# Optimization experiments

Measured on AMD Instinct MI355X. Metric: run time of the kernel, lower is better.

## Reference

```python
import jax, jax.numpy as jnp
import numpy as np

N, E = 16384, 262144
NS_N, NV_N = 128, 64      # node irreps: 128x0e + 64x1o
NS_E, NV_E = 64, 32       # edge irreps: 64x0e + 32x1o
C_OH, LAT = 16, 128
DS, DV = 128, 64          # irreps_out: 128x0e + 64x1o
GS = DS + DV              # gate input scalars (128 act scalars + 64 gates)
SC = 2 * NS_N + NS_E      # 320 concatenated scalar channels
VC = 2 * NV_N + NV_E      # 160 concatenated l=1 channels
M0_IN = SC + VC           # 480 m=0 features into SO2 linear
M0_OUT = GS + DV          # 256 m=0 outputs
AVG_NEI = 16.0
EPS = 1e-8


def setup_inputs() -> dict:
    key = jax.random.key(0)
    ks = jax.random.split(key, 20)
    f = lambda k, s: jax.random.normal(k, s, dtype=jnp.float32)
    return dict(
        node_feat=f(ks[0], (N, NS_N + 3 * NV_N)),
        edge_feat=f(ks[1], (E, NS_E + 3 * NV_E)),
        edge_vec=f(ks[2], (E, 3)),
        latents=f(ks[3], (E, LAT)),
        node_onehot=jax.nn.one_hot(jax.random.randint(ks[4], (N,), 0, C_OH), C_OH, dtype=jnp.float32),
        ln_n_g0=jnp.ones(NS_N), ln_n_b0=jnp.zeros(NS_N), ln_n_g1=jnp.ones(NV_N),
        ln_e_g0=jnp.ones(NS_E), ln_e_b0=jnp.zeros(NS_E), ln_e_g1=jnp.ones(NV_E),
        W_m0=f(ks[5], (M0_IN, M0_OUT)),
        w_r=f(ks[6], (VC, DV)), w_i=f(ks[7], (VC, DV)),
        W_env=f(ks[8], (LAT, DS + DV)),
        Wp0=f(ks[9], (DS, DS)), bp0=jnp.zeros(DS), Wpv=f(ks[10], (DV, DV)),
        Wtp0=f(ks[11], (DS, C_OH, GS)), Wtp1=f(ks[12], (DV, C_OH, DV)),
        Wo0=f(ks[13], (DS, DS)), bo0=jnp.zeros(DS), Wov=f(ks[14], (DV, DV)),
        res_param=jnp.zeros(()),
        edge_index=jax.random.randint(ks[15], (2, E), 0, N),
    )


def _sep_ln(s, v, g0, b0, g1):
    # separable equivariant layer norm: LN on scalars, per-sample RMS on l=1 block
    mu = s.mean(-1, keepdims=True)
    var = jnp.mean((s - mu) ** 2, -1, keepdims=True)
    s = (s - mu) * jax.lax.rsqrt(var + EPS) * g0 + b0
    vvar = jnp.mean(v * v, axis=(-2, -1), keepdims=True)  # component norm, degree-balanced (single l=1)
    v = v * jax.lax.rsqrt(vvar + EPS) * g1[None, :, None]
    return s, v


def _edge_frame(vec):
    # orthonormal frame (a, e1, e2) with a along the edge
    a = vec * jax.lax.rsqrt(jnp.sum(vec * vec, -1, keepdims=True) + EPS)
    helper = jnp.where(jnp.abs(a[:, 2:3]) < 0.99,
                       jnp.array([0.0, 0.0, 1.0], dtype=vec.dtype),
                       jnp.array([1.0, 0.0, 0.0], dtype=vec.dtype))
    e1 = jnp.cross(helper, a)
    e1 = e1 * jax.lax.rsqrt(jnp.sum(e1 * e1, -1, keepdims=True) + EPS)
    e2 = jnp.cross(a, e1)
    return a, e1, e2


def reference(node_feat, edge_feat, edge_vec, latents, node_onehot,
              ln_n_g0, ln_n_b0, ln_n_g1, ln_e_g0, ln_e_b0, ln_e_g1,
              W_m0, w_r, w_i, W_env, Wp0, bp0, Wpv,
              Wtp0, Wtp1, Wo0, bo0, Wov, res_param, edge_index):
    src, dst = edge_index[0], edge_index[1]
    ns, nv = node_feat[:, :NS_N], node_feat[:, NS_N:].reshape(-1, NV_N, 3)
    es, ev = edge_feat[:, :NS_E], edge_feat[:, NS_E:].reshape(-1, NV_E, 3)
    ns, nv = _sep_ln(ns, nv, ln_n_g0, ln_n_b0, ln_n_g1)
    es, ev = _sep_ln(es, ev, ln_e_g0, ln_e_b0, ln_e_g1)
    # per-edge concat: node[src] + edge + node[dst]
    s_cat = jnp.concatenate([ns[src], es, ns[dst]], -1)          # [E, SC]
    v_cat = jnp.concatenate([nv[src], ev, nv[dst]], 1)           # [E, VC, 3]
    # SO2 linear: rotate into edge frame, mix per |m|, rotate back
    a, e1, e2 = _edge_frame(edge_vec)
    c0 = jnp.einsum('eci,ei->ec', v_cat, a)
    c1 = jnp.einsum('eci,ei->ec', v_cat, e1)
    c2 = jnp.einsum('eci,ei->ec', v_cat, e2)
    m0 = jnp.concatenate([s_cat, c0], -1) @ W_m0 * (1.0 / np.sqrt(M0_IN))  # [E, M0_OUT]
    s_out, c0o = m0[:, :GS], m0[:, GS:]
    inv = 1.0 / np.sqrt(VC)
    c1o = (c1 @ w_r - c2 @ w_i) * inv
    c2o = (c1 @ w_i + c2 @ w_r) * inv
    v_out = (c0o[..., None] * a[:, None, :] + c1o[..., None] * e1[:, None, :]
             + c2o[..., None] * e2[:, None, :])                  # [E, DV, 3]
    # gate activation
    s_act = jax.nn.silu(s_out[:, :DS])
    gates = jax.nn.sigmoid(s_out[:, DS:])
    v_g = v_out * gates[..., None]
    # lin_post (per-l linear, scalar bias)
    s2 = s_act @ Wp0 * (1.0 / np.sqrt(DS)) + bp0
    v2 = jnp.einsum('eui,uv->evi', v_g, Wpv) * (1.0 / np.sqrt(DV))
    # env weighting from latents (E3ElementLinear, per-irrep-channel scalars)
    w = latents @ W_env * (1.0 / np.sqrt(LAT))
    s2 = s2 * w[:, :DS]
    v2 = v2 * w[:, DS:, None]
    nrm = 1.0 / np.sqrt(AVG_NEI)
    sa = jax.ops.segment_sum(s2, dst, num_segments=N) * nrm
    va = jax.ops.segment_sum(v2, dst, num_segments=N) * nrm
    # one-hot FullyConnectedTensorProduct (in2 all 0e) + gate + linear
    t0 = jnp.einsum('nu,nc,ucv->nv', sa, node_onehot, Wtp0) * (1.0 / np.sqrt(DS * C_OH))
    t1 = jnp.einsum('nui,nc,ucv->nvi', va, node_onehot, Wtp1) * (1.0 / np.sqrt(DV * C_OH))
    s3 = jax.nn.silu(t0[:, :DS])
    v3 = t1 * jax.nn.sigmoid(t0[:, DS:])[..., None]
    s4 = s3 @ Wo0 * (1.0 / np.sqrt(DS)) + bo0
    v4 = jnp.einsum('nui,uv->nvi', v3, Wov) * (1.0 / np.sqrt(DV))
    new = jnp.concatenate([s4, v4.reshape(-1, 3 * DV)], -1)
    r = jax.nn.sigmoid(res_param)
    return r * node_feat + (1.0 - r) * new
```

## Files before the change

### kernel.cpp

```cpp
#include <hip/hip_runtime.h>
#include <math.h>

#define N_NODES 16384
#define N_EDGES 262144
#define EPSF 1e-8f

#define OFF_X     0
#define OFF_C12   31232
#define OFF_LAT   52224
#define OFF_FR    60928
#define OFF_EDST  62464
#define OFF_WENV  62592
#define POOL_BYTES 75392
#define OFF_SACT  0
#define OFF_GATE  8704
#define OFF_C0O   17408
#define OFF_C1O   31232
#define OFF_C2O   39936
#define OFF_VG    8704

typedef __bf16 bf16x8 __attribute__((ext_vector_type(8)));
typedef float  f32x4  __attribute__((ext_vector_type(4)));

__device__ __forceinline__ f32x4 MFMA16(bf16x8 a, bf16x8 b, f32x4 c){
  return __builtin_amdgcn_mfma_f32_16x16x32_bf16(a, b, c, 0, 0, 0);
}

__device__ __forceinline__ unsigned short f2bf(float x){
  union { float f; unsigned u; } c; c.f = x;
  unsigned u = c.u;
  u += 0x7FFFu + ((u>>16)&1u);
  return (unsigned short)(u>>16);
}
__device__ __forceinline__ float bf2f(unsigned short h){
  union { unsigned u; float f; } c; c.u = ((unsigned)h)<<16;
  return c.f;
}
__device__ __forceinline__ float wsum64(float v){
  #pragma unroll
  for (int m=1; m<64; m<<=1) v += __shfl_xor(v, m);
  return v;
}
__device__ __forceinline__ float wsum32(float v){
  #pragma unroll
  for (int m=1; m<32; m<<=1) v += __shfl_xor(v, m);
  return v;
}
__device__ __forceinline__ float sigm(float x){ return 1.0f/(1.0f+__expf(-x)); }
__device__ __forceinline__ float silu(float x){ return x/(1.0f+__expf(-x)); }

__global__ __launch_bounds__(256) void k_pack(const float* __restrict__ src,
                                              unsigned short* __restrict__ dst,
                                              int K, int N){
  int i = blockIdx.x*256 + threadIdx.x;
  if (i >= K*N) return;
  int k = i / N, n = i - k*N;
  int idx = (((k>>5)*N + n)*4 + ((k>>3)&3))*8 + (k&7);
  dst[idx] = f2bf(src[i]);
}
__global__ __launch_bounds__(256) void k_pack_wc(const float* __restrict__ wr,
                                                 const float* __restrict__ wi,
                                                 unsigned short* __restrict__ dst){
  int i = blockIdx.x*256 + threadIdx.x;
  if (i >= 320*128) return;
  int k = i >> 7, n = i & 127;
  float v;
  if (k < 160) v = (n < 64) ? wr[k*64 + n]        : wi[k*64 + (n-64)];
  else         v = (n < 64) ? -wi[(k-160)*64 + n] : wr[(k-160)*64 + (n-64)];
  int idx = (((k>>5)*128 + n)*4 + ((k>>3)&3))*8 + (k&7);
  dst[idx] = f2bf(v);
}

__global__ __launch_bounds__(256) void k_hist(const int* __restrict__ eidx, int* __restrict__ cnt){
  int e = blockIdx.x*256 + threadIdx.x;
  if (e < N_EDGES) atomicAdd(&cnt[eidx[N_EDGES+e]], 1);
}
__global__ __launch_bounds__(256) void k_scan(const int* __restrict__ cnt,
                                              int* __restrict__ rowp, int* __restrict__ cursor){
  __shared__ int part[256];
  __shared__ int pref[257];
  const int t = threadIdx.x;
  const int base = t*64;
  int s = 0;
  for (int i=0;i<64;i++) s += cnt[base+i];
  part[t] = s; __syncthreads();
  if (t==0){ int a=0; for (int i=0;i<256;i++){ pref[i]=a; a+=part[i]; } pref[256]=a; }
  __syncthreads();
  int a = pref[t];
  for (int i=0;i<64;i++){ rowp[base+i]=a; cursor[base+i]=a; a += cnt[base+i]; }
  if (t==0) rowp[N_NODES] = pref[256];
}
__global__ __launch_bounds__(256) void k_fill(const int* __restrict__ eidx,
                                              int* __restrict__ cursor, int* __restrict__ perm){
  int e = blockIdx.x*256 + threadIdx.x;
  if (e < N_EDGES){
    int pos = atomicAdd(&cursor[eidx[N_EDGES+e]], 1);
    perm[pos] = e;
  }
}

__global__ __launch_bounds__(256) void k_node_ln(
    const float* __restrict__ nf, const float* __restrict__ g0,
    const float* __restrict__ b0, const float* __restrict__ g1,
    float* __restrict__ ns_ln, float* __restrict__ nv_ln)
{
  const int tid  = threadIdx.x;
  const int lane = tid & 63;
  const int n    = blockIdx.x*4 + (tid>>6);
  const float* row = nf + (size_t)n*320;

  float s0 = row[lane], s1 = row[64+lane];
  float mu = wsum64(s0+s1) * (1.0f/128.0f);
  float d0 = s0-mu, d1 = s1-mu;
  float var = wsum64(d0*d0+d1*d1) * (1.0f/128.0f);
  float rs = rsqrtf(var + EPSF);
  ns_ln[(size_t)n*128 + lane]      = d0*rs*g0[lane]    + b0[lane];
  ns_ln[(size_t)n*128 + 64+lane]   = d1*rs*g0[64+lane] + b0[64+lane];

  float px = row[128+lane*3+0], py = row[128+lane*3+1], pz = row[128+lane*3+2];
  float vvar = wsum64(px*px+py*py+pz*pz) * (1.0f/192.0f);
  float vsc = rsqrtf(vvar + EPSF) * g1[lane];
  nv_ln[(size_t)n*192 + lane*3+0] = px*vsc;
  nv_ln[(size_t)n*192 + lane*3+1] = py*vsc;
  nv_ln[(size_t)n*192 + lane*3+2] = pz*vsc;
}

__global__ __launch_bounds__(256,2) void k_edge(
  const float* __restrict__ ef, const float* __restrict__ evec,
  const float* __restrict__ lats,
  const float* __restrict__ g0e, const float* __restrict__ b0e, const float* __restrict__ g1e,
  const unsigned short* __restrict__ pWm0, const unsigned short* __restrict__ pWc,
  const unsigned short* __restrict__ pWenv, const unsigned short* __restrict__ pWp0,
  const unsigned short* __restrict__ pWpv,
  const float* __restrict__ bp0,
  const int* __restrict__ eidx,
  const float* __restrict__ ns_ln, const float* __restrict__ nv_ln,
  float* __restrict__ sa, float* __restrict__ va,
  _Float16* __restrict__ msg, int use_msg)
{
  extern __shared__ unsigned char pool[];
  const int tid = threadIdx.x;
  unsigned short* Xs   = (unsigned short*)(pool + OFF_X);
  unsigned short* C12s = (unsigned short*)(pool + OFF_C12);
  unsigned short* LTs  = (unsigned short*)(pool + OFF_LAT);
  float* FRf = (float*)(pool + OFF_FR);
  int*   EDST = (int*)(pool + OFF_EDST);
  unsigned short* WEs = (unsigned short*)(pool + OFF_WENV);

  {
    const int ln = tid & 31;
    for (int eo=0; eo<4; ++eo){
      const int el = eo*8 + (tid>>5);
      const size_t ge = (size_t)blockIdx.x*32 + el;
      const int src = eidx[ge];
      const int dst = eidx[N_EDGES + ge];

      float vx=evec[ge*3+0], vy=evec[ge*3+1], vz=evec[ge*3+2];
      float rn = rsqrtf(vx*vx+vy*vy+vz*vz+EPSF);
      float ax=vx*rn, ay=vy*rn, az=vz*rn;
      float hx, hz;
      if (fabsf(az) < 0.99f){ hx=0.f; hz=1.f; } else { hx=1.f; hz=0.f; }
      float e1x = -hz*ay;
      float e1y = hz*ax - hx*az;
      float e1z = hx*ay;
      float rn1 = rsqrtf(e1x*e1x+e1y*e1y+e1z*e1z+EPSF);
      e1x*=rn1; e1y*=rn1; e1z*=rn1;
      float e2x = ay*e1z - az*e1y;
      float e2y = az*e1x - ax*e1z;
      float e2z = ax*e1y - ay*e1x;
      if (ln==0){
        FRf[el*12+0]=ax;  FRf[el*12+1]=ay;  FRf[el*12+2]=az;
        FRf[el*12+3]=e1x; FRf[el*12+4]=e1y; FRf[el*12+5]=e1z;
        FRf[el*12+6]=e2x; FRf[el*12+7]=e2y; FRf[el*12+8]=e2z;
        EDST[el]=dst;
      }

      const float* erow = ef + ge*160;
      float s0=erow[ln], s1=erow[32+ln];
      float mu = wsum32(s0+s1)*(1.f/64.f);
      float d0=s0-mu, d1=s1-mu;
      float var = wsum32(d0*d0+d1*d1)*(1.f/64.f);
      float rs = rsqrtf(var+EPSF);
      Xs[el*488 + 128+ln] = f2bf(d0*rs*g0e[ln]    + b0e[ln]);
      Xs[el*488 + 160+ln] = f2bf(d1*rs*g0e[32+ln] + b0e[32+ln]);

      float wx=erow[64+ln*3+0], wy=erow[64+ln*3+1], wz=erow[64+ln*3+2];
      float vvar = wsum32(wx*wx+wy*wy+wz*wz)*(1.f/96.f);
      float vsc = rsqrtf(vvar+EPSF)*g1e[ln];
      wx*=vsc; wy*=vsc; wz*=vsc;
      Xs  [el*488 + 320+64+ln]   = f2bf(wx*ax +wy*ay +wz*az);
      C12s[el*328 + 64+ln]       = f2bf(wx*e1x+wy*e1y+wz*e1z);
      C12s[el*328 + 160+64+ln]   = f2bf(wx*e2x+wy*e2y+wz*e2z);

      const float* nss = ns_ln + (size_t)src*128;
      const float* nsd = ns_ln + (size_t)dst*128;
      #pragma unroll
      for (int q=0;q<4;q++){
        int idx=ln+32*q;
        Xs[el*488 + idx]     = f2bf(nss[idx]);
        Xs[el*488 + 192+idx] = f2bf(nsd[idx]);
      }

      const float* nvs = nv_ln + (size_t)src*192;
      const float* nvd = nv_ln + (size_t)dst*192;
      #pragma unroll
      for (int q=0;q<2;q++){
        int u = ln+32*q;
        float px=nvs[u*3+0], py=nvs[u*3+1], pz=nvs[u*3+2];
        Xs  [el*488 + 320+u]     = f2bf(px*ax +py*ay +pz*az);
        C12s[el*328 + u]         = f2bf(px*e1x+py*e1y+pz*e1z);
        C12s[el*328 + 160+u]     = f2bf(px*e2x+py*e2y+pz*e2z);
        px=nvd[u*3+0]; py=nvd[u*3+1]; pz=nvd[u*3+2];
        Xs  [el*488 + 320+96+u]  = f2bf(px*ax +py*ay +pz*az);
        C12s[el*328 + 96+u]      = f2bf(px*e1x+py*e1y+pz*e1z);
        C12s[el*328 + 160+96+u]  = f2bf(px*e2x+py*e2y+pz*e2z);
      }

      #pragma unroll
      for (int q=0;q<4;q++){ int k=ln+32*q; LTs[el*136+k] = f2bf(lats[ge*128+k]); }
    }
  }
  __syncthreads();

  const int wid = tid>>6, l = tid&63;
  const int r15 = l&15, g = l>>4;
  const f32x4 zero4 = {0.f,0.f,0.f,0.f};

  f32x4 acc1[2][4], acc2[2][2], acc3[2][3];
  #pragma unroll
  for (int m=0;m<2;m++){
    #pragma unroll
    for (int n=0;n<4;n++) acc1[m][n]=zero4;
    #pragma unroll
    for (int n=0;n<2;n++) acc2[m][n]=zero4;
    #pragma unroll
    for (int n=0;n<3;n++) acc3[m][n]=zero4;
  }

  for (int kc=0;kc<15;kc++){
    bf16x8 a0 = *(const bf16x8*)&Xs[(    r15)*488 + kc*32 + g*8];
    bf16x8 a1 = *(const bf16x8*)&Xs[(16+ r15)*488 + kc*32 + g*8];
    const unsigned short* bp = pWm0 + ((size_t)(kc*256 + wid*64 + r15)*4 + g)*8;
    #pragma unroll
    for (int n=0;n<4;n++){
      bf16x8 b = *(const bf16x8*)(bp + n*512);
      acc1[0][n] = MFMA16(a0,b,acc1[0][n]);
      acc1[1][n] = MFMA16(a1,b,acc1[1][n]);
    }
  }
  for (int kc=0;kc<10;kc++){
    bf16x8 a0 = *(const bf16x8*)&C12s[(    r15)*328 + kc*32 + g*8];
    bf16x8 a1 = *(const bf16x8*)&C12s[(16+ r15)*328 + kc*32 + g*8];
    const unsigned short* bp = pWc + ((size_t)(kc*128 + wid*32 + r15)*4 + g)*8;
    #pragma unroll
    for (int n=0;n<2;n++){
      bf16x8 b = *(const bf16x8*)(bp + n*512);
      acc2[0][n] = MFMA16(a0,b,acc2[0][n]);
      acc2[1][n] = MFMA16(a1,b,acc2[1][n]);
    }
  }
  for (int kc=0;kc<4;kc++){
    bf16x8 a0 = *(const bf16x8*)&LTs[(    r15)*136 + kc*32 + g*8];
    bf16x8 a1 = *(const bf16x8*)&LTs[(16+ r15)*136 + kc*32 + g*8];
    const unsigned short* bp = pWenv + ((size_t)(kc*192 + wid*48 + r15)*4 + g)*8;
    #pragma unroll
    for (int n=0;n<3;n++){
      bf16x8 b = *(const bf16x8*)(bp + n*512);
      acc3[0][n] = MFMA16(a0,b,acc3[0][n]);
      acc3[1][n] = MFMA16(a1,b,acc3[1][n]);
    }
  }

  #pragma unroll
  for (int m=0;m<2;m++)
    #pragma unroll
    for (int n=0;n<3;n++)
      #pragma unroll
      for (int r=0;r<4;r++){
        int e = m*16 + g*4 + r;
        int j = wid*48 + n*16 + r15;
        WEs[e*200 + j] = f2bf(acc3[m][n][r]*0.08838834764831845f);
      }

  __syncthreads();

  {
    unsigned short* SAs = (unsigned short*)(pool + OFF_SACT);
    float* GAf = (float*)(pool + OFF_GATE);
    float* C0f = (float*)(pool + OFF_C0O);
    #pragma unroll
    for (int m=0;m<2;m++)
      #pragma unroll
      for (int n=0;n<4;n++)
        #pragma unroll
        for (int r=0;r<4;r++){
          int e = m*16 + g*4 + r;
          int j = wid*64 + n*16 + r15;
          float v = acc1[m][n][r]*0.04564354645876384f;
          if (j < 128)      SAs[e*136 + j] = f2bf(silu(v));
          else if (j < 192) GAf[e*68 + (j-128)] = sigm(v);
          else              C0f[e*68 + (j-192)] = v;
        }
    float* C1f = (float*)(pool + OFF_C1O);
    float* C2f = (float*)(pool + OFF_C2O);
    #pragma unroll
    for (int m=0;m<2;m++)
      #pragma unroll
      for (int n=0;n<2;n++)
        #pragma unroll
        for (int r=0;r<4;r++){
          int e = m*16 + g*4 + r;
          int j = wid*32 + n*16 + r15;
          float v = acc2[m][n][r]*0.07905694150420949f;
          if (j < 64) C1f[e*68 + j] = v;
          else        C2f[e*68 + (j-64)] = v;
        }
  }
  __syncthreads();

  {
    const int e = tid>>3, u0 = (tid&7)*8;
    const float* GAf = (const float*)(pool + OFF_GATE);
    const float* C0f = (const float*)(pool + OFF_C0O);
    const float* C1f = (const float*)(pool + OFF_C1O);
    const float* C2f = (const float*)(pool + OFF_C2O);
    float ax=FRf[e*12+0],  ay=FRf[e*12+1],  az=FRf[e*12+2];
    float b1x=FRf[e*12+3], b1y=FRf[e*12+4], b1z=FRf[e*12+5];
    float b2x=FRf[e*12+6], b2y=FRf[e*12+7], b2z=FRf[e*12+8];
    float vgx[8], vgy[8], vgz[8];
    #pragma unroll
    for (int i=0;i<8;i++){
      int u = u0+i;
      float gt = GAf[e*68+u];
      float c0 = C0f[e*68+u], c1 = C1f[e*68+u], c2 = C2f[e*68+u];
      vgx[i] = (c0*ax + c1*b1x + c2*b2x)*gt;
      vgy[i] = (c0*ay + c1*b1y + c2*b2y)*gt;
      vgz[i] = (c0*az + c1*b1z + c2*b2z)*gt;
    }
    __syncthreads();
    unsigned short* VGs = (unsigned short*)(pool + OFF_VG);
    #pragma unroll
    for (int i=0;i<8;i++){
      VGs[0*2304 + e*72 + u0+i] = f2bf(vgx[i]);
      VGs[1*2304 + e*72 + u0+i] = f2bf(vgy[i]);
      VGs[2*2304 + e*72 + u0+i] = f2bf(vgz[i]);
    }
  }
  __syncthreads();

  {
    const unsigned short* SAs = (const unsigned short*)(pool + OFF_SACT);
    const unsigned short* VGs = (const unsigned short*)(pool + OFF_VG);
    f32x4 acc4[2][2], acc5[3][2];
    #pragma unroll
    for (int m=0;m<2;m++){ acc4[m][0]=zero4; acc4[m][1]=zero4; }
    #pragma unroll
    for (int c=0;c<3;c++){ acc5[c][0]=zero4; acc5[c][1]=zero4; }

    for (int kc=0;kc<4;kc++){
      bf16x8 a0 = *(const bf16x8*)&SAs[(    r15)*136 + kc*32 + g*8];
      bf16x8 a1 = *(const bf16x8*)&SAs[(16+ r15)*136 + kc*32 + g*8];
      const unsigned short* bp = pWp0 + ((size_t)(kc*128 + wid*32 + r15)*4 + g)*8;
      #pragma unroll
      for (int n=0;n<2;n++){
        bf16x8 b = *(const bf16x8*)(bp + n*512);
        acc4[0][n] = MFMA16(a0,b,acc4[0][n]);
        acc4[1][n] = MFMA16(a1,b,acc4[1][n]);
      }
    }
    #pragma unroll
    for (int c=0;c<3;c++){
      #pragma unroll
      for (int kc=0;kc<2;kc++){
        bf16x8 a0 = *(const bf16x8*)&VGs[c*2304 + (    r15)*72 + kc*32 + g*8];
        bf16x8 a1 = *(const bf16x8*)&VGs[c*2304 + (16+ r15)*72 + kc*32 + g*8];
        bf16x8 b  = *(const bf16x8*)(pWpv + ((size_t)(kc*64 + wid*16 + r15)*4 + g)*8);
        acc5[c][0] = MFMA16(a0,b,acc5[c][0]);
        acc5[c][1] = MFMA16(a1,b,acc5[c][1]);
      }
    }

    if (use_msg){
      const size_t gebase = (size_t)blockIdx.x*32;
      #pragma unroll
      for (int m=0;m<2;m++)
        #pragma unroll
        for (int n=0;n<2;n++)
          #pragma unroll
          for (int r=0;r<4;r++){
            int e = m*16 + g*4 + r;
            int j = wid*32 + n*16 + r15;
            float v = acc4[m][n][r]*0.08838834764831845f + bp0[j];
            v *= bf2f(WEs[e*200 + j]);
            msg[(gebase+e)*320 + j] = (_Float16)v;
          }
      #pragma unroll
      for (int c=0;c<3;c++)
        #pragma unroll
        for (int m=0;m<2;m++)
          #pragma unroll
          for (int r=0;r<4;r++){
            int e = m*16 + g*4 + r;
            int vch = wid*16 + r15;
            float val = acc5[c][m][r]*0.125f * bf2f(WEs[e*200 + 128 + vch]);
            msg[(gebase+e)*320 + 128 + c*64 + vch] = (_Float16)val;
          }
    } else {
      #pragma unroll
      for (int m=0;m<2;m++)
        #pragma unroll
        for (int n=0;n<2;n++)
          #pragma unroll
          for (int r=0;r<4;r++){
            int e = m*16 + g*4 + r;
            int j = wid*32 + n*16 + r15;
            float v = acc4[m][n][r]*0.08838834764831845f + bp0[j];
            v *= bf2f(WEs[e*200 + j]);
            atomicAdd(&sa[(size_t)EDST[e]*128 + j], v);
          }
      #pragma unroll
      for (int c=0;c<3;c++)
        #pragma unroll
        for (int m=0;m<2;m++)
          #pragma unroll
          for (int r=0;r<4;r++){
            int e = m*16 + g*4 + r;
            int vch = wid*16 + r15;
            float val = acc5[c][m][r]*0.125f * bf2f(WEs[e*200 + 128 + vch]);
            atomicAdd(&va[(size_t)EDST[e]*192 + vch*3 + c], val);
          }
    }
  }
}

__global__ __launch_bounds__(256) void k_node_out(
  const float* __restrict__ nf, const float* __restrict__ oh,
  const float* __restrict__ Wtp0, const float* __restrict__ Wtp1,
  const float* __restrict__ Wo0, const float* __restrict__ bo0,
  const float* __restrict__ Wov, const float* __restrict__ resp,
  const float* __restrict__ sa, const float* __restrict__ va,
  const _Float16* __restrict__ msg, const int* __restrict__ rowp,
  const int* __restrict__ perm, int use_msg,
  float* __restrict__ out)
{
  __shared__ float SAB[4][128];
  __shared__ float VX[4][64], VY[4][64], VZ[4][64];
  __shared__ float S3 [4][128];
  __shared__ float V3 [4][256];
  const int tid=threadIdx.x, lane=tid&63, g=tid>>6;
  const int n = blockIdx.x*4 + g;

  float cf=0.f;
  #pragma unroll
  for (int j=0;j<16;j++) cf += j*oh[(size_t)n*16+j];
  const int c = (int)(cf+0.5f);

  if (use_msg){
    float a0=0.f,a1=0.f,vx=0.f,vy=0.f,vz=0.f;
    const int beg = rowp[n], end = rowp[n+1];
    for (int i=beg;i<end;++i){
      const _Float16* mr = msg + (size_t)perm[i]*320;
      a0 += (float)mr[lane];
      a1 += (float)mr[64+lane];
      vx += (float)mr[128+lane];
      vy += (float)mr[192+lane];
      vz += (float)mr[256+lane];
    }
    SAB[g][lane]    = a0*0.25f;
    SAB[g][64+lane] = a1*0.25f;
    VX[g][lane]=vx*0.25f; VY[g][lane]=vy*0.25f; VZ[g][lane]=vz*0.25f;
  } else {
    SAB[g][lane]    = sa[(size_t)n*128+lane]   *0.25f;
    SAB[g][64+lane] = sa[(size_t)n*128+64+lane]*0.25f;
    VX[g][lane] = va[(size_t)n*192+lane*3+0]*0.25f;
    VY[g][lane] = va[(size_t)n*192+lane*3+1]*0.25f;
    VZ[g][lane] = va[(size_t)n*192+lane*3+2]*0.25f;
  }
  __syncthreads();

  float t00=0.f, t01=0.f, t02=0.f;
  const float* w0c = Wtp0 + (size_t)c*192;
  for (int u=0;u<128;u++){
    float s = SAB[g][u];
    t00 += s * w0c[(size_t)u*3072 + lane];
    t01 += s * w0c[(size_t)u*3072 + lane+64];
    t02 += s * w0c[(size_t)u*3072 + lane+128];
  }
  const float sct0 = 0.02209708691f;
  t00*=sct0; t01*=sct0; t02*=sct0;

  float t1x=0.f,t1y=0.f,t1z=0.f;
  const float* w1c = Wtp1 + (size_t)c*64;
  for (int u=0;u<64;u++){
    float wv = w1c[(size_t)u*1024 + lane];
    t1x += VX[g][u]*wv;
    t1y += VY[g][u]*wv;
    t1z += VZ[g][u]*wv;
  }
  t1x*=0.03125f; t1y*=0.03125f; t1z*=0.03125f;

  S3[g][lane]    = silu(t00);
  S3[g][64+lane] = silu(t01);
  float g2 = sigm(t02);
  float4 v3v = {t1x*g2, t1y*g2, t1z*g2, 0.f};
  *(float4*)&V3[g][lane*4] = v3v;
  __syncthreads();

  float s40=0.f, s41=0.f;
  for (int k=0;k<128;k++){
    float s3k = S3[g][k];
    s40 += s3k*Wo0[k*128+lane];
    s41 += s3k*Wo0[k*128+64+lane];
  }
  s40 = s40*0.08838834765f + bo0[lane];
  s41 = s41*0.08838834765f + bo0[64+lane];

  float v4x=0.f,v4y=0.f,v4z=0.f;
  for (int u=0;u<64;u++){
    float4 v3u = *(const float4*)&V3[g][u*4];
    float wv = Wov[u*64+lane];
    v4x += v3u.x*wv; v4y += v3u.y*wv; v4z += v3u.z*wv;
  }
  v4x*=0.125f; v4y*=0.125f; v4z*=0.125f;

  const float r = sigm(resp[0]);
  const float* row = nf + (size_t)n*320;
  float* orow = out + (size_t)n*320;
  orow[lane]      = r*row[lane]      + (1.f-r)*s40;
  orow[64+lane]   = r*row[64+lane]   + (1.f-r)*s41;
  orow[128+lane*3+0] = r*row[128+lane*3+0] + (1.f-r)*v4x;
  orow[128+lane*3+1] = r*row[128+lane*3+1] + (1.f-r)*v4y;
  orow[128+lane*3+2] = r*row[128+lane*3+2] + (1.f-r)*v4z;
}

extern "C" void kernel_launch(void* const* d_in, const int* in_sizes, int n_in,
                              void* d_out, int out_size, void* d_ws, size_t ws_size,
                              hipStream_t stream)
{
  const float* nf   = (const float*)d_in[0];
  const float* ef   = (const float*)d_in[1];
  const float* evec = (const float*)d_in[2];
  const float* lats = (const float*)d_in[3];
  const float* oh   = (const float*)d_in[4];
  const float* g0n  = (const float*)d_in[5];
  const float* b0n  = (const float*)d_in[6];
  const float* g1n  = (const float*)d_in[7];
  const float* g0e  = (const float*)d_in[8];
  const float* b0e  = (const float*)d_in[9];
  const float* g1e  = (const float*)d_in[10];
  const float* Wm0  = (const float*)d_in[11];
  const float* wr   = (const float*)d_in[12];
  const float* wi   = (const float*)d_in[13];
  const float* Wenv = (const float*)d_in[14];
  const float* Wp0  = (const float*)d_in[15];
  const float* bp0  = (const float*)d_in[16];
  const float* Wpv  = (const float*)d_in[17];
  const float* Wtp0 = (const float*)d_in[18];
  const float* Wtp1 = (const float*)d_in[19];
  const float* Wo0  = (const float*)d_in[20];
  const float* bo0  = (const float*)d_in[21];
  const float* Wov  = (const float*)d_in[22];
  const float* resp = (const float*)d_in[23];
  const int*   eidx = (const int*)d_in[24];

  float* ws    = (float*)d_ws;
  float* ns_ln = ws;
  float* nv_ln = ws + (size_t)N_NODES*128;
  float* sa    = ws + (size_t)N_NODES*320;
  float* va    = ws + (size_t)N_NODES*448;
  unsigned short* wpk = (unsigned short*)(ws + (size_t)N_NODES*640);
  unsigned short* pWm0  = wpk;
  unsigned short* pWc   = wpk + 122880;
  unsigned short* pWenv = wpk + 163840;
  unsigned short* pWp0  = wpk + 188416;
  unsigned short* pWpv  = wpk + 204800;
  int* ibuf   = (int*)(ws + (size_t)N_NODES*640 + 104448);
  int* cnt    = ibuf;
  int* rowp   = ibuf + 16384;
  int* cursor = ibuf + 32769;
  int* perm   = ibuf + 49153;
  _Float16* msg = (_Float16*)(ws + (size_t)N_NODES*640 + 104448 + 311304);

  const size_t need = ((size_t)N_NODES*640 + 104448 + 311304)*4 + (size_t)N_EDGES*320*2;
  const int use_msg = (ws_size >= need) ? 1 : 0;

  k_pack<<<(122880+255)/256, 256, 0, stream>>>(Wm0,  pWm0, 480, 256);
  k_pack_wc<<<(40960+255)/256, 256, 0, stream>>>(wr, wi, pWc);
  k_pack<<<(24576+255)/256, 256, 0, stream>>>(Wenv, pWenv, 128, 192);
  k_pack<<<(16384+255)/256, 256, 0, stream>>>(Wp0,  pWp0, 128, 128);
  k_pack<<<(4096+255)/256,  256, 0, stream>>>(Wpv,  pWpv, 64, 64);
  k_node_ln<<<N_NODES/4, 256, 0, stream>>>(nf, g0n, b0n, g1n, ns_ln, nv_ln);

  if (use_msg){
    hipMemsetAsync(cnt, 0, N_NODES*sizeof(int), stream);
    k_hist<<<(N_EDGES+255)/256, 256, 0, stream>>>(eidx, cnt);
    k_scan<<<1, 256, 0, stream>>>(cnt, rowp, cursor);
    k_fill<<<(N_EDGES+255)/256, 256, 0, stream>>>(eidx, cursor, perm);
  } else {
    hipMemsetAsync(sa, 0, (size_t)N_NODES*320*sizeof(float), stream);
  }

  k_edge<<<N_EDGES/32, 256, POOL_BYTES, stream>>>(ef, evec, lats, g0e, b0e, g1e,
                                                  pWm0, pWc, pWenv, pWp0, pWpv, bp0,
                                                  eidx, ns_ln, nv_ln, sa, va, msg, use_msg);
  k_node_out<<<N_NODES/4, 256, 0, stream>>>(nf, oh, Wtp0, Wtp1, Wo0, bo0, Wov,
                                            resp, sa, va, msg, rowp, perm, use_msg,
                                            (float*)d_out);
}
```

Before: 681.5 us.

## Process edges in dst-sorted order with segmented atomic reduction and split env GEMM

Edges are now visited in destination-sorted order via the CSR permutation, and each block reduces runs of equal destinations in shared memory before issuing float atomics, replacing the fp16 message buffer and gather pass in the node kernel. The latent-to-envelope GEMM moves into a separate kernel writing a bf16 per-edge weight buffer, which shrinks k_edge's LDS so it can run three blocks per CU. Node scalar LN output is stored as bf16 for vectorized gathers, and weight B-fragments are software-prefetched in the main GEMM loops. This adds an extra kernel and a global wbuf round trip, and accumulation order now depends on atomics.

```diff
diff --git a/kernel.cpp b/kernel.cpp
--- a/kernel.cpp
+++ b/kernel.cpp
@@ -7,11 +7,9 @@
 
 #define OFF_X     0
 #define OFF_C12   31232
-#define OFF_LAT   52224
-#define OFF_FR    60928
-#define OFF_EDST  62464
-#define OFF_WENV  62592
-#define POOL_BYTES 75392
+#define OFF_FR    52224
+#define OFF_EDST  53760
+#define POOL_BYTES 53888
 #define OFF_SACT  0
 #define OFF_GATE  8704
 #define OFF_C0O   17408
@@ -102,7 +100,7 @@
 __global__ __launch_bounds__(256) void k_node_ln(
     const float* __restrict__ nf, const float* __restrict__ g0,
     const float* __restrict__ b0, const float* __restrict__ g1,
-    float* __restrict__ ns_ln, float* __restrict__ nv_ln)
+    unsigned short* __restrict__ ns_ln, float* __restrict__ nv_ln)
 {
   const int tid  = threadIdx.x;
   const int lane = tid & 63;
@@ -114,8 +112,8 @@
   float d0 = s0-mu, d1 = s1-mu;
   float var = wsum64(d0*d0+d1*d1) * (1.0f/128.0f);
   float rs = rsqrtf(var + EPSF);
-  ns_ln[(size_t)n*128 + lane]      = d0*rs*g0[lane]    + b0[lane];
-  ns_ln[(size_t)n*128 + 64+lane]   = d1*rs*g0[64+lane] + b0[64+lane];
+  ns_ln[(size_t)n*128 + lane]    = f2bf(d0*rs*g0[lane]    + b0[lane]);
+  ns_ln[(size_t)n*128 + 64+lane] = f2bf(d1*rs*g0[64+lane] + b0[64+lane]);
 
   float px = row[128+lane*3+0], py = row[128+lane*3+1], pz = row[128+lane*3+2];
   float vvar = wsum64(px*px+py*py+pz*pz) * (1.0f/192.0f);
@@ -125,37 +123,90 @@
   nv_ln[(size_t)n*192 + lane*3+2] = pz*vsc;
 }
 
-__global__ __launch_bounds__(256,2) void k_edge(
+__global__ __launch_bounds__(256) void k_wenv(
+  const float* __restrict__ lats, const unsigned short* __restrict__ pWenv,
+  const int* __restrict__ perm, unsigned short* __restrict__ wbuf)
+{
+  __shared__ unsigned short A[64*136];
+  const int tid = threadIdx.x;
+  {
+    const int row = tid>>2, part = tid&3;
+    const int slot = blockIdx.x*64 + row;
+    const int e = perm[slot];
+    const float* lr = lats + (size_t)e*128 + part*32;
+    #pragma unroll
+    for (int q=0;q<8;q++){
+      float4 v = *(const float4*)(lr + q*4);
+      int cb = part*32 + q*4;
+      A[row*136 + cb+0] = f2bf(v.x);
+      A[row*136 + cb+1] = f2bf(v.y);
+      A[row*136 + cb+2] = f2bf(v.z);
+      A[row*136 + cb+3] = f2bf(v.w);
+    }
+  }
+  __syncthreads();
+  const int wid = tid>>6, l = tid&63, r15 = l&15, g = l>>4;
+  const f32x4 zero4 = {0.f,0.f,0.f,0.f};
+  f32x4 acc[4][3];
+  #pragma unroll
+  for (int m=0;m<4;m++)
+    #pragma unroll
+    for (int n=0;n<3;n++) acc[m][n]=zero4;
+
+  const unsigned short* bbase = pWenv + ((size_t)(wid*48 + r15)*4 + g)*8;
+  #pragma unroll
+  for (int kc=0;kc<4;kc++){
+    bf16x8 b[3];
+    #pragma unroll
+    for (int n=0;n<3;n++) b[n] = *(const bf16x8*)(bbase + (size_t)kc*6144 + n*512);
+    #pragma unroll
+    for (int m=0;m<4;m++){
+      bf16x8 a = *(const bf16x8*)&A[(m*16+r15)*136 + kc*32 + g*8];
+      #pragma unroll
+      for (int n=0;n<3;n++) acc[m][n] = MFMA16(a, b[n], acc[m][n]);
+    }
+  }
+  #pragma unroll
+  for (int m=0;m<4;m++)
+    #pragma unroll
+    for (int n=0;n<3;n++)
+      #pragma unroll
+      for (int r=0;r<4;r++){
+        int sr = m*16 + g*4 + r;
+        int j  = wid*48 + n*16 + r15;
+        wbuf[(size_t)(blockIdx.x*64 + sr)*192 + j] = f2bf(acc[m][n][r]*0.08838834764831845f);
+      }
+}
+
+__global__ __launch_bounds__(256,3) void k_edge(
   const float* __restrict__ ef, const float* __restrict__ evec,
-  const float* __restrict__ lats,
   const float* __restrict__ g0e, const float* __restrict__ b0e, const float* __restrict__ g1e,
   const unsigned short* __restrict__ pWm0, const unsigned short* __restrict__ pWc,
-  const unsigned short* __restrict__ pWenv, const unsigned short* __restrict__ pWp0,
-  const unsigned short* __restrict__ pWpv,
+  const unsigned short* __restrict__ pWp0, const unsigned short* __restrict__ pWpv,
   const float* __restrict__ bp0,
-  const int* __restrict__ eidx,
-  const float* __restrict__ ns_ln, const float* __restrict__ nv_ln,
-  float* __restrict__ sa, float* __restrict__ va,
-  _Float16* __restrict__ msg, int use_msg)
+  const int* __restrict__ eidx, const int* __restrict__ perm,
+  const unsigned short* __restrict__ ns_ln, const float* __restrict__ nv_ln,
+  const unsigned short* __restrict__ wbuf,
+  float* __restrict__ sa, float* __restrict__ va)
 {
   extern __shared__ unsigned char pool[];
   const int tid = threadIdx.x;
   unsigned short* Xs   = (unsigned short*)(pool + OFF_X);
   unsigned short* C12s = (unsigned short*)(pool + OFF_C12);
-  unsigned short* LTs  = (unsigned short*)(pool + OFF_LAT);
   float* FRf = (float*)(pool + OFF_FR);
   int*   EDST = (int*)(pool + OFF_EDST);
-  unsigned short* WEs = (unsigned short*)(pool + OFF_WENV);
 
   {
     const int ln = tid & 31;
+    #pragma unroll
     for (int eo=0; eo<4; ++eo){
       const int el = eo*8 + (tid>>5);
-      const size_t ge = (size_t)blockIdx.x*32 + el;
-      const int src = eidx[ge];
-      const int dst = eidx[N_EDGES + ge];
-
-      float vx=evec[ge*3+0], vy=evec[ge*3+1], vz=evec[ge*3+2];
+      const int slot = blockIdx.x*32 + el;
+      const size_t e = (size_t)perm[slot];
+      const int src = eidx[e];
+      const int dst = eidx[N_EDGES + e];
+
+      float vx=evec[e*3+0], vy=evec[e*3+1], vz=evec[e*3+2];
       float rn = rsqrtf(vx*vx+vy*vy+vz*vz+EPSF);
       float ax=vx*rn, ay=vy*rn, az=vz*rn;
       float hx, hz;
@@ -175,7 +226,7 @@
         EDST[el]=dst;
       }
 
-      const float* erow = ef + ge*160;
+      const float* erow = ef + e*160;
       float s0=erow[ln], s1=erow[32+ln];
       float mu = wsum32(s0+s1)*(1.f/64.f);
       float d0=s0-mu, d1=s1-mu;
@@ -192,14 +243,10 @@
       C12s[el*328 + 64+ln]       = f2bf(wx*e1x+wy*e1y+wz*e1z);
       C12s[el*328 + 160+64+ln]   = f2bf(wx*e2x+wy*e2y+wz*e2z);
 
-      const float* nss = ns_ln + (size_t)src*128;
-      const float* nsd = ns_ln + (size_t)dst*128;
-      #pragma unroll
-      for (int q=0;q<4;q++){
-        int idx=ln+32*q;
-        Xs[el*488 + idx]     = f2bf(nss[idx]);
-        Xs[el*488 + 192+idx] = f2bf(nsd[idx]);
-      }
+      const unsigned short* nss = ns_ln + (size_t)src*128;
+      const unsigned short* nsd = ns_ln + (size_t)dst*128;
+      *(uint2*)&Xs[el*488 + ln*4]       = *(const uint2*)&nss[ln*4];
+      *(uint2*)&Xs[el*488 + 192 + ln*4] = *(const uint2*)&nsd[ln*4];
 
       const float* nvs = nv_ln + (size_t)src*192;
       const float* nvd = nv_ln + (size_t)dst*192;
@@ -215,9 +262,6 @@
         C12s[el*328 + 96+u]      = f2bf(px*e1x+py*e1y+pz*e1z);
         C12s[el*328 + 160+96+u]  = f2bf(px*e2x+py*e2y+pz*e2z);
       }
-
-      #pragma unroll
-      for (int q=0;q<4;q++){ int k=ln+32*q; LTs[el*136+k] = f2bf(lats[ge*128+k]); }
     }
   }
   __syncthreads();
@@ -226,61 +270,61 @@
   const int r15 = l&15, g = l>>4;
   const f32x4 zero4 = {0.f,0.f,0.f,0.f};
 
-  f32x4 acc1[2][4], acc2[2][2], acc3[2][3];
+  f32x4 acc1[2][4], acc2[2][2];
   #pragma unroll
   for (int m=0;m<2;m++){
     #pragma unroll
     for (int n=0;n<4;n++) acc1[m][n]=zero4;
     #pragma unroll
     for (int n=0;n<2;n++) acc2[m][n]=zero4;
-    #pragma unroll
-    for (int n=0;n<3;n++) acc3[m][n]=zero4;
-  }
-
-  for (int kc=0;kc<15;kc++){
-    bf16x8 a0 = *(const bf16x8*)&Xs[(    r15)*488 + kc*32 + g*8];
-    bf16x8 a1 = *(const bf16x8*)&Xs[(16+ r15)*488 + kc*32 + g*8];
-    const unsigned short* bp = pWm0 + ((size_t)(kc*256 + wid*64 + r15)*4 + g)*8;
-    #pragma unroll
-    for (int n=0;n<4;n++){
-      bf16x8 b = *(const bf16x8*)(bp + n*512);
-      acc1[0][n] = MFMA16(a0,b,acc1[0][n]);
-      acc1[1][n] = MFMA16(a1,b,acc1[1][n]);
-    }
-  }
-  for (int kc=0;kc<10;kc++){
-    bf16x8 a0 = *(const bf16x8*)&C12s[(    r15)*328 + kc*32 + g*8];
-    bf16x8 a1 = *(const bf16x8*)&C12s[(16+ r15)*328 + kc*32 + g*8];
-    const unsigned short* bp = pWc + ((size_t)(kc*128 + wid*32 + r15)*4 + g)*8;
-    #pragma unroll
-    for (int n=0;n<2;n++){
-      bf16x8 b = *(const bf16x8*)(bp + n*512);
-      acc2[0][n] = MFMA16(a0,b,acc2[0][n]);
-      acc2[1][n] = MFMA16(a1,b,acc2[1][n]);
-    }
-  }
-  for (int kc=0;kc<4;kc++){
-    bf16x8 a0 = *(const bf16x8*)&LTs[(    r15)*136 + kc*32 + g*8];
-    bf16x8 a1 = *(const bf16x8*)&LTs[(16+ r15)*136 + kc*32 + g*8];
-    const unsigned short* bp = pWenv + ((size_t)(kc*192 + wid*48 + r15)*4 + g)*8;
-    #pragma unroll
-    for (int n=0;n<3;n++){
-      bf16x8 b = *(const bf16x8*)(bp + n*512);
-      acc3[0][n] = MFMA16(a0,b,acc3[0][n]);
-      acc3[1][n] = MFMA16(a1,b,acc3[1][n]);
-    }
-  }
-
-  #pragma unroll
-  for (int m=0;m<2;m++)
-    #pragma unroll
-    for (int n=0;n<3;n++)
-      #pragma unroll
-      for (int r=0;r<4;r++){
-        int e = m*16 + g*4 + r;
-        int j = wid*48 + n*16 + r15;
-        WEs[e*200 + j] = f2bf(acc3[m][n][r]*0.08838834764831845f);
-      }
+  }
+
+  {
+    const unsigned short* bbase = pWm0 + ((size_t)(wid*64 + r15)*4 + g)*8;
+    bf16x8 bc[4];
+    #pragma unroll
+    for (int n=0;n<4;n++) bc[n] = *(const bf16x8*)(bbase + n*512);
+    for (int kc=0;kc<15;kc++){
+      bf16x8 a0 = *(const bf16x8*)&Xs[(    r15)*488 + kc*32 + g*8];
+      bf16x8 a1 = *(const bf16x8*)&Xs[(16+ r15)*488 + kc*32 + g*8];
+      bf16x8 bn[4];
+      if (kc<14){
+        const unsigned short* np = bbase + (size_t)(kc+1)*8192;
+        #pragma unroll
+        for (int n=0;n<4;n++) bn[n] = *(const bf16x8*)(np + n*512);
+      }
+      #pragma unroll
+      for (int n=0;n<4;n++){
+        acc1[0][n] = MFMA16(a0,bc[n],acc1[0][n]);
+        acc1[1][n] = MFMA16(a1,bc[n],acc1[1][n]);
+      }
+      #pragma unroll
+      for (int n=0;n<4;n++) bc[n]=bn[n];
+    }
+  }
+  {
+    const unsigned short* bbase = pWc + ((size_t)(wid*32 + r15)*4 + g)*8;
+    bf16x8 bc[2];
+    #pragma unroll
+    for (int n=0;n<2;n++) bc[n] = *(const bf16x8*)(bbase + n*512);
+    for (int kc=0;kc<10;kc++){
+      bf16x8 a0 = *(const bf16x8*)&C12s[(    r15)*328 + kc*32 + g*8];
+      bf16x8 a1 = *(const bf16x8*)&C12s[(16+ r15)*328 + kc*32 + g*8];
+      bf16x8 bn[2];
+      if (kc<9){
+        const unsigned short* np = bbase + (size_t)(kc+1)*4096;
+        #pragma unroll
+        for (int n=0;n<2;n++) bn[n] = *(const bf16x8*)(np + n*512);
+      }
+      #pragma unroll
+      for (int n=0;n<2;n++){
+        acc2[0][n] = MFMA16(a0,bc[n],acc2[0][n]);
+        acc2[1][n] = MFMA16(a1,bc[n],acc2[1][n]);
+      }
+      #pragma unroll
+      for (int n=0;n<2;n++) bc[n]=bn[n];
+    }
+  }
 
   __syncthreads();
 
@@ -351,84 +395,96 @@
   {
     const unsigned short* SAs = (const unsigned short*)(pool + OFF_SACT);
     const unsigned short* VGs = (const unsigned short*)(pool + OFF_VG);
+    const int sbase = blockIdx.x*32;
+
+    float wsc[2][2][4], wvc[2][4], bp0v[2];
+    #pragma unroll
+    for (int n=0;n<2;n++) bp0v[n] = bp0[wid*32 + n*16 + r15];
+    #pragma unroll
+    for (int m=0;m<2;m++)
+      #pragma unroll
+      for (int r=0;r<4;r++){
+        int e = m*16 + g*4 + r;
+        #pragma unroll
+        for (int n=0;n<2;n++)
+          wsc[m][n][r] = bf2f(wbuf[(size_t)(sbase+e)*192 + wid*32 + n*16 + r15]);
+        wvc[m][r] = bf2f(wbuf[(size_t)(sbase+e)*192 + 128 + wid*16 + r15]);
+      }
+
     f32x4 acc4[2][2], acc5[3][2];
     #pragma unroll
     for (int m=0;m<2;m++){ acc4[m][0]=zero4; acc4[m][1]=zero4; }
     #pragma unroll
     for (int c=0;c<3;c++){ acc5[c][0]=zero4; acc5[c][1]=zero4; }
 
-    for (int kc=0;kc<4;kc++){
-      bf16x8 a0 = *(const bf16x8*)&SAs[(    r15)*136 + kc*32 + g*8];
-      bf16x8 a1 = *(const bf16x8*)&SAs[(16+ r15)*136 + kc*32 + g*8];
-      const unsigned short* bp = pWp0 + ((size_t)(kc*128 + wid*32 + r15)*4 + g)*8;
-      #pragma unroll
-      for (int n=0;n<2;n++){
-        bf16x8 b = *(const bf16x8*)(bp + n*512);
-        acc4[0][n] = MFMA16(a0,b,acc4[0][n]);
-        acc4[1][n] = MFMA16(a1,b,acc4[1][n]);
-      }
-    }
-    #pragma unroll
-    for (int c=0;c<3;c++){
-      #pragma unroll
-      for (int kc=0;kc<2;kc++){
-        bf16x8 a0 = *(const bf16x8*)&VGs[c*2304 + (    r15)*72 + kc*32 + g*8];
-        bf16x8 a1 = *(const bf16x8*)&VGs[c*2304 + (16+ r15)*72 + kc*32 + g*8];
-        bf16x8 b  = *(const bf16x8*)(pWpv + ((size_t)(kc*64 + wid*16 + r15)*4 + g)*8);
-        acc5[c][0] = MFMA16(a0,b,acc5[c][0]);
-        acc5[c][1] = MFMA16(a1,b,acc5[c][1]);
-      }
-    }
-
-    if (use_msg){
-      const size_t gebase = (size_t)blockIdx.x*32;
+    {
+      const unsigned short* bbase = pWp0 + ((size_t)(wid*32 + r15)*4 + g)*8;
+      #pragma unroll
+      for (int kc=0;kc<4;kc++){
+        bf16x8 a0 = *(const bf16x8*)&SAs[(    r15)*136 + kc*32 + g*8];
+        bf16x8 a1 = *(const bf16x8*)&SAs[(16+ r15)*136 + kc*32 + g*8];
+        #pragma unroll
+        for (int n=0;n<2;n++){
+          bf16x8 b = *(const bf16x8*)(bbase + (size_t)kc*4096 + n*512);
+          acc4[0][n] = MFMA16(a0,b,acc4[0][n]);
+          acc4[1][n] = MFMA16(a1,b,acc4[1][n]);
+        }
+      }
+    }
+    {
+      bf16x8 b5[2];
+      #pragma unroll
+      for (int kc=0;kc<2;kc++)
+        b5[kc] = *(const bf16x8*)(pWpv + ((size_t)(kc*64 + wid*16 + r15)*4 + g)*8);
+      #pragma unroll
+      for (int c=0;c<3;c++)
+        #pragma unroll
+        for (int kc=0;kc<2;kc++){
+          bf16x8 a0 = *(const bf16x8*)&VGs[c*2304 + (    r15)*72 + kc*32 + g*8];
+          bf16x8 a1 = *(const bf16x8*)&VGs[c*2304 + (16+ r15)*72 + kc*32 + g*8];
+          acc5[c][0] = MFMA16(a0,b5[kc],acc5[c][0]);
+          acc5[c][1] = MFMA16(a1,b5[kc],acc5[c][1]);
+        }
+    }
+
+    __syncthreads();
+    float* R = (float*)pool;
+    #pragma unroll
+    for (int m=0;m<2;m++)
+      #pragma unroll
+      for (int n=0;n<2;n++)
+        #pragma unroll
+        for (int r=0;r<4;r++){
+          int e = m*16 + g*4 + r;
+          int j = wid*32 + n*16 + r15;
+          R[e*320 + j] = (acc4[m][n][r]*0.08838834764831845f + bp0v[n]) * wsc[m][n][r];
+        }
+    #pragma unroll
+    for (int c=0;c<3;c++)
       #pragma unroll
       for (int m=0;m<2;m++)
         #pragma unroll
-        for (int n=0;n<2;n++)
-          #pragma unroll
-          for (int r=0;r<4;r++){
-            int e = m*16 + g*4 + r;
-            int j = wid*32 + n*16 + r15;
-            float v = acc4[m][n][r]*0.08838834764831845f + bp0[j];
-            v *= bf2f(WEs[e*200 + j]);
-            msg[(gebase+e)*320 + j] = (_Float16)v;
-          }
-      #pragma unroll
-      for (int c=0;c<3;c++)
-        #pragma unroll
-        for (int m=0;m<2;m++)
-          #pragma unroll
-          for (int r=0;r<4;r++){
-            int e = m*16 + g*4 + r;
-            int vch = wid*16 + r15;
-            float val = acc5[c][m][r]*0.125f * bf2f(WEs[e*200 + 128 + vch]);
-            msg[(gebase+e)*320 + 128 + c*64 + vch] = (_Float16)val;
-          }
-    } else {
-      #pragma unroll
-      for (int m=0;m<2;m++)
-        #pragma unroll
-        for (int n=0;n<2;n++)
-          #pragma unroll
-          for (int r=0;r<4;r++){
-            int e = m*16 + g*4 + r;
-            int j = wid*32 + n*16 + r15;
-            float v = acc4[m][n][r]*0.08838834764831845f + bp0[j];
-            v *= bf2f(WEs[e*200 + j]);
-            atomicAdd(&sa[(size_t)EDST[e]*128 + j], v);
-          }
-      #pragma unroll
-      for (int c=0;c<3;c++)
-        #pragma unroll
-        for (int m=0;m<2;m++)
-          #pragma unroll
-          for (int r=0;r<4;r++){
-            int e = m*16 + g*4 + r;
-            int vch = wid*16 + r15;
-            float val = acc5[c][m][r]*0.125f * bf2f(WEs[e*200 + 128 + vch]);
-            atomicAdd(&va[(size_t)EDST[e]*192 + vch*3 + c], val);
-          }
+        for (int r=0;r<4;r++){
+          int e = m*16 + g*4 + r;
+          int vch = wid*16 + r15;
+          R[e*320 + 128 + vch*3 + c] = acc5[c][m][r]*0.125f * wvc[m][r];
+        }
+    __syncthreads();
+
+    for (int j = tid; j < 320; j += 256){
+      float accv = R[j];
+      int cur = EDST[0];
+      for (int e=1;e<32;e++){
+        int d = EDST[e];
+        float v = R[e*320 + j];
+        if (d != cur){
+          float* tgt = (j<128) ? &sa[(size_t)cur*128 + j] : &va[(size_t)cur*192 + (j-128)];
+          atomicAdd(tgt, accv);
+          accv = v; cur = d;
+        } else accv += v;
+      }
+      float* tgt = (j<128) ? &sa[(size_t)cur*128 + j] : &va[(size_t)cur*192 + (j-128)];
+      atomicAdd(tgt, accv);
     }
   }
 }
@@ -439,8 +495,6 @@
   const float* __restrict__ Wo0, const float* __restrict__ bo0,
   const float* __restrict__ Wov, const float* __restrict__ resp,
   const float* __restrict__ sa, const float* __restrict__ va,
-  const _Float16* __restrict__ msg, const int* __restrict__ rowp,
-  const int* __restrict__ perm, int use_msg,
   float* __restrict__ out)
 {
   __shared__ float SAB[4][128];
@@ -455,27 +509,11 @@
   for (int j=0;j<16;j++) cf += j*oh[(size_t)n*16+j];
   const int c = (int)(cf+0.5f);
 
-  if (use_msg){
-    float a0=0.f,a1=0.f,vx=0.f,vy=0.f,vz=0.f;
-    const int beg = rowp[n], end = rowp[n+1];
-    for (int i=beg;i<end;++i){
-      const _Float16* mr = msg + (size_t)perm[i]*320;
-      a0 += (float)mr[lane];
-      a1 += (float)mr[64+lane];
-      vx += (float)mr[128+lane];
-      vy += (float)mr[192+lane];
-      vz += (float)mr[256+lane];
-    }
-    SAB[g][lane]    = a0*0.25f;
-    SAB[g][64+lane] = a1*0.25f;
-    VX[g][lane]=vx*0.25f; VY[g][lane]=vy*0.25f; VZ[g][lane]=vz*0.25f;
-  } else {
-    SAB[g][lane]    = sa[(size_t)n*128+lane]   *0.25f;
-    SAB[g][64+lane] = sa[(size_t)n*128+64+lane]*0.25f;
-    VX[g][lane] = va[(size_t)n*192+lane*3+0]*0.25f;
-    VY[g][lane] = va[(size_t)n*192+lane*3+1]*0.25f;
-    VZ[g][lane] = va[(size_t)n*192+lane*3+2]*0.25f;
-  }
+  SAB[g][lane]    = sa[(size_t)n*128+lane]   *0.25f;
+  SAB[g][64+lane] = sa[(size_t)n*128+64+lane]*0.25f;
+  VX[g][lane] = va[(size_t)n*192+lane*3+0]*0.25f;
+  VY[g][lane] = va[(size_t)n*192+lane*3+1]*0.25f;
+  VZ[g][lane] = va[(size_t)n*192+lane*3+2]*0.25f;
   __syncthreads();
 
   float t00=0.f, t01=0.f, t02=0.f;
@@ -563,26 +601,26 @@
   const float* resp = (const float*)d_in[23];
   const int*   eidx = (const int*)d_in[24];
 
-  float* ws    = (float*)d_ws;
-  float* ns_ln = ws;
-  float* nv_ln = ws + (size_t)N_NODES*128;
-  float* sa    = ws + (size_t)N_NODES*320;
-  float* va    = ws + (size_t)N_NODES*448;
-  unsigned short* wpk = (unsigned short*)(ws + (size_t)N_NODES*640);
+  char* base = (char*)d_ws;
+  unsigned short* ns_ln = (unsigned short*)(base);
+  float* nv_ln = (float*)(base + 4194304);
+  float* sa    = (float*)(base + 16777216);
+  float* va    = (float*)(base + 25165824);
+  unsigned short* wpk = (unsigned short*)(base + 37748736);
   unsigned short* pWm0  = wpk;
   unsigned short* pWc   = wpk + 122880;
   unsigned short* pWenv = wpk + 163840;
   unsigned short* pWp0  = wpk + 188416;
   unsigned short* pWpv  = wpk + 204800;
-  int* ibuf   = (int*)(ws + (size_t)N_NODES*640 + 104448);
+  int* ibuf   = (int*)(base + 38166528);
   int* cnt    = ibuf;
   int* rowp   = ibuf + 16384;
   int* cursor = ibuf + 32769;
   int* perm   = ibuf + 49153;
-  _Float16* msg = (_Float16*)(ws + (size_t)N_NODES*640 + 104448 + 311304);
-
-  const size_t need = ((size_t)N_NODES*640 + 104448 + 311304)*4 + (size_t)N_EDGES*320*2;
-  const int use_msg = (ws_size >= need) ? 1 : 0;
+  unsigned short* wbuf = (unsigned short*)(base + 39411720);
+
+  hipMemsetAsync(sa, 0, (size_t)N_NODES*320*sizeof(float), stream);
+  hipMemsetAsync(cnt, 0, N_NODES*sizeof(int), stream);
 
   k_pack<<<(122880+255)/256, 256, 0, stream>>>(Wm0,  pWm0, 480, 256);
   k_pack_wc<<<(40960+255)/256, 256, 0, stream>>>(wr, wi, pWc);
@@ -591,19 +629,16 @@
   k_pack<<<(4096+255)/256,  256, 0, stream>>>(Wpv,  pWpv, 64, 64);
   k_node_ln<<<N_NODES/4, 256, 0, stream>>>(nf, g0n, b0n, g1n, ns_ln, nv_ln);
 
-  if (use_msg){
-    hipMemsetAsync(cnt, 0, N_NODES*sizeof(int), stream);
-    k_hist<<<(N_EDGES+255)/256, 256, 0, stream>>>(eidx, cnt);
-    k_scan<<<1, 256, 0, stream>>>(cnt, rowp, cursor);
-    k_fill<<<(N_EDGES+255)/256, 256, 0, stream>>>(eidx, cursor, perm);
-  } else {
-    hipMemsetAsync(sa, 0, (size_t)N_NODES*320*sizeof(float), stream);
-  }
-
-  k_edge<<<N_EDGES/32, 256, POOL_BYTES, stream>>>(ef, evec, lats, g0e, b0e, g1e,
-                                                  pWm0, pWc, pWenv, pWp0, pWpv, bp0,
-                                                  eidx, ns_ln, nv_ln, sa, va, msg, use_msg);
+  k_hist<<<(N_EDGES+255)/256, 256, 0, stream>>>(eidx, cnt);
+  k_scan<<<1, 256, 0, stream>>>(cnt, rowp, cursor);
+  k_fill<<<(N_EDGES+255)/256, 256, 0, stream>>>(eidx, cursor, perm);
+
+  k_wenv<<<N_EDGES/64, 256, 0, stream>>>(lats, pWenv, perm, wbuf);
+
+  k_edge<<<N_EDGES/32, 256, POOL_BYTES, stream>>>(ef, evec, g0e, b0e, g1e,
+                                                  pWm0, pWc, pWp0, pWpv, bp0,
+                                                  eidx, perm, ns_ln, nv_ln, wbuf,
+                                                  sa, va);
   k_node_out<<<N_NODES/4, 256, 0, stream>>>(nf, oh, Wtp0, Wtp1, Wo0, bo0, Wov,
-                                            resp, sa, va, msg, rowp, perm, use_msg,
-                                            (float*)d_out);
-}
+                                            resp, sa, va, (float*)d_out);
+}
```

Result: no change. 686.1 us (+0.7%).
